# Performance work log

Measured on AMD Instinct MI355X. Metric: run time of the kernel, lower is better.

Reference implementation:

```python
import jax, jax.numpy as jnp
import numpy as np

THETA0 = 3.0
THETA = 5.0


def _edt(bg):
    """Exact Euclidean distance transform.
    bg: [B,H,W] bool, True where distance is 0 (the 'background'/feature set).
    Returns [B,H,W] float32 distance of every pixel to the nearest True pixel.
    Separable two-pass algorithm: 1D pass along H via scan, then exact
    min over column offsets along W (Meijster lower-envelope done densely).
    """
    B, H, W = bg.shape
    big = jnp.float32(H + W)
    f = bg.astype(jnp.float32)
    xs = jnp.moveaxis(f, 1, 0)  # [H,B,W] scan over rows

    def step(carry, row):
        d = jnp.where(row > 0, 0.0, carry + 1.0)
        return d, d

    init = jnp.full((B, W), big, jnp.float32)
    _, gf = jax.lax.scan(step, init, xs)                  # top-down
    _, gb = jax.lax.scan(step, init, xs, reverse=True)    # bottom-up
    g = jnp.minimum(gf, gb)            # [H,B,W] 1D vertical distance
    g = jnp.moveaxis(g, 0, 1)          # [B,H,W]
    g2 = jnp.minimum(g, big) ** 2
    col = jnp.arange(W, dtype=jnp.float32)
    off2 = (col[:, None] - col[None, :]) ** 2             # [j,k]
    # d2[b,i,j] = min_k g2[b,i,k] + (j-k)^2   -> [B,H,W,W] intermediate
    d2 = jnp.min(g2[:, :, None, :] + off2[None, None, :, :], axis=-1)
    return jnp.sqrt(d2)


def reference(predictions, targets):
    # predictions: [B,1,H,W] logits; targets: [B,1,H,W] binary masks
    t = targets[:, 0]                                   # [B,H,W]
    fg = t > 0.5
    dist_pos = _edt(~fg)   # distance_transform_edt(target): dist to nearest 0
    dist_neg = _edt(fg)    # distance_transform_edt(1-target): dist to nearest 1
    dist_map = jnp.where(fg, dist_pos, -dist_neg)
    # weight = 1 / (1 + exp((|d| - theta0)/theta)) == sigmoid(-(|d|-theta0)/theta)
    weight = jax.nn.sigmoid(-(jnp.abs(dist_map) - THETA0) / THETA)[:, None]  # [B,1,H,W]
    # numerically stable BCE-with-logits == BCE(sigmoid(x), t)
    x = predictions
    bce = jnp.maximum(x, 0.0) - x * targets + jnp.log1p(jnp.exp(-jnp.abs(x)))
    return jnp.mean(bce * weight)


def setup_inputs() -> dict:
    key = jax.random.key(0)
    k1, k2 = jax.random.split(key)
    B, C, H, W = 8, 1, 256, 256
    predictions = jax.random.normal(k1, (B, C, H, W), dtype=jnp.float32)
    targets = jax.random.randint(k2, (B, C, H, W), 0, 2).astype(jnp.float32)
    return {"predictions": predictions, "targets": targets}
```

## Files before the change

### kernel.cpp

```cpp
#include <hip/hip_runtime.h>
#include <math.h>

#define BB 8
#define HH 256
#define WW 256
#define NPIX (BB*HH*WW)
#define BIGF 512.0f
#define INF9 1e9f

#define P_OFF   (2 * NPIX)
#define P_STRIDE 32
#define C_OFF   (P_OFF + 16 * P_STRIDE)

__device__ __forceinline__ void col_scan_g2(bool f0, bool f1, bool f2, bool f3,
                                            int lane, float g2[4]) {
  float d = INF9;
  d = f0 ? 0.0f : d + 1.0f; float lf0 = d;
  d = f1 ? 0.0f : d + 1.0f; float lf1 = d;
  d = f2 ? 0.0f : d + 1.0f; float lf2 = d;
  d = f3 ? 0.0f : d + 1.0f; float lf3 = d;
  float F = lf3;
#pragma unroll
  for (int s = 1; s < 64; s <<= 1) {
    float u = __shfl_up(F, s, 64) + 4.0f * (float)s;
    if (lane >= s) F = fminf(F, u);
  }
  float Fe = __shfl_up(F, 1, 64);
  if (lane == 0) Fe = INF9;

  d = INF9;
  d = f3 ? 0.0f : d + 1.0f; float lb3 = d;
  d = f2 ? 0.0f : d + 1.0f; float lb2 = d;
  d = f1 ? 0.0f : d + 1.0f; float lb1 = d;
  d = f0 ? 0.0f : d + 1.0f; float lb0 = d;
  float Bv = lb0;
#pragma unroll
  for (int s = 1; s < 64; s <<= 1) {
    float u = __shfl_down(Bv, s, 64) + 4.0f * (float)s;
    if (lane < 64 - s) Bv = fminf(Bv, u);
  }
  float Be = __shfl_down(Bv, 1, 64);
  if (lane == 63) Be = INF9;

  float v0 = fminf(fminf(lf0, Fe + 1.0f), fminf(lb0, Be + 4.0f));
  float v1 = fminf(fminf(lf1, Fe + 2.0f), fminf(lb1, Be + 3.0f));
  float v2 = fminf(fminf(lf2, Fe + 3.0f), fminf(lb2, Be + 2.0f));
  float v3 = fminf(fminf(lf3, Fe + 4.0f), fminf(lb3, Be + 1.0f));
  v0 = fminf(v0, BIGF); v1 = fminf(v1, BIGF);
  v2 = fminf(v2, BIGF); v3 = fminf(v3, BIGF);
  g2[0] = v0 * v0; g2[1] = v1 * v1; g2[2] = v2 * v2; g2[3] = v3 * v3;
}

__global__ __launch_bounds__(256) void edt_vertical2(
    const float* __restrict__ tgt,
    float* __restrict__ ws) {
  if (blockIdx.x == 0) {
    if (threadIdx.x < 16) ws[P_OFF + threadIdx.x * P_STRIDE] = 0.0f;
    if (threadIdx.x == 16) ((int*)ws)[C_OFF] = 0;
  }

  float* gA2 = ws;
  float* gB2 = ws + NPIX;

  int wid = (blockIdx.x * 256 + threadIdx.x) >> 6;
  int lane = threadIdx.x & 63;
  int b = wid >> 8;
  int w = wid & 255;
  size_t ibase = (size_t)b * HH * WW + w;

  float t0 = tgt[ibase + (size_t)(4 * lane + 0) * WW];
  float t1 = tgt[ibase + (size_t)(4 * lane + 1) * WW];
  float t2 = tgt[ibase + (size_t)(4 * lane + 2) * WW];
  float t3 = tgt[ibase + (size_t)(4 * lane + 3) * WW];
  bool g0 = t0 > 0.5f, g1 = t1 > 0.5f, g2b = t2 > 0.5f, g3 = t3 > 0.5f;

  float a2[4], b2[4];
  col_scan_g2(!g0, !g1, !g2b, !g3, lane, a2);
  col_scan_g2(g0, g1, g2b, g3, lane, b2);

#pragma unroll
  for (int k = 0; k < 4; ++k) {
    size_t o = ibase + (size_t)(4 * lane + k) * WW;
    gA2[o] = a2[k];
    gB2[o] = b2[k];
  }
}

#define ENV_GROUP(kk) { float4 v = s4[kk];                        \
    float D0 = fw - (float)(4 * (kk));                            \
    d2 = fminf(d2, fmaf(D0, D0, v.x));                            \
    float D1 = D0 - 1.0f; d2 = fminf(d2, fmaf(D1, D1, v.y));      \
    float D2 = D0 - 2.0f; d2 = fminf(d2, fmaf(D2, D2, v.z));      \
    float D3 = D0 - 3.0f; d2 = fminf(d2, fmaf(D3, D3, v.w)); }

__global__ __launch_bounds__(1024) void edt_row_loss3(
    const float* __restrict__ pred,
    const float* __restrict__ tgt,
    float* __restrict__ ws,
    float* __restrict__ out) {
  __shared__ __align__(16) float lA[4][WW];
  __shared__ __align__(16) float lB[4][WW];
  __shared__ float wsum[16];
  __shared__ int lastFlag;

  const float* gA2 = ws;
  const float* gB2 = ws + NPIX;
  float* partials = ws + P_OFF;
  int* counter = ((int*)ws) + C_OFF;

  int tid = threadIdx.x;
  size_t base = (size_t)blockIdx.x * (4 * WW);

  ((float*)lA)[tid] = gA2[base + tid];
  ((float*)lB)[tid] = gB2[base + tid];
  float x = pred[base + tid];
  float t = tgt[base + tid];
  __syncthreads();

  int r = tid >> 8;
  int w = tid & 255;
  bool fg = t > 0.5f;
  const float4* s4 = (const float4*)(fg ? lA[r] : lB[r]);

  int w0 = w & ~63;
  int kc0 = w0 >> 2;
  float fw = (float)w;
  float d2 = 1e30f;

#pragma unroll 4
  for (int k = kc0; k < kc0 + 16; ++k) ENV_GROUP(k);

  int kL = kc0 - 1;
  int kR = kc0 + 16;
  for (int iter = 0; iter < 16; ++iter) {
    int bL = (kL >= 0) ? (w0 - 4 * kL - 3) : 100000;
    int bR = (kR <= 63) ? (4 * kR - w0 - 63) : 100000;
    int bb = min(bL, bR);
    float bb2 = (float)bb * (float)bb;
    if (__all(d2 <= bb2)) break;
    if (kL >= 0) { ENV_GROUP(kL); kL--; }
    if (kR <= 63) { ENV_GROUP(kR); kR++; }
  }

  float dd = sqrtf(d2);
  float weight = 1.0f / (1.0f + __expf((dd - 3.0f) * 0.2f));
  float bce = fmaxf(x, 0.0f) - x * t + log1pf(__expf(-fabsf(x)));
  float c = bce * weight * (1.0f / (float)NPIX);

#pragma unroll
  for (int off = 32; off > 0; off >>= 1) c += __shfl_down(c, off, 64);
  if ((tid & 63) == 0) wsum[tid >> 6] = c;
  __syncthreads();

  if (tid < 64) {
    float v = (tid < 16) ? wsum[tid] : 0.0f;
#pragma unroll
    for (int off = 8; off > 0; off >>= 1) v += __shfl_down(v, off, 64);
    if (tid == 0) {
      atomicAdd(&partials[(blockIdx.x & 15) * P_STRIDE], v);
      __threadfence();
      int done = atomicAdd(counter, 1);
      lastFlag = (done == (int)gridDim.x - 1) ? 1 : 0;
    }
  }
  __syncthreads();

  if (lastFlag && tid < 64) {
    float v = (tid < 16) ? atomicAdd(&partials[tid * P_STRIDE], 0.0f) : 0.0f;
#pragma unroll
    for (int off = 8; off > 0; off >>= 1) v += __shfl_down(v, off, 64);
    if (tid == 0) out[0] = v;
  }
}

extern "C" void kernel_launch(void* const* d_in, const int* in_sizes, int n_in,
                              void* d_out, int out_size, void* d_ws, size_t ws_size,
                              hipStream_t stream) {
  const float* pred = (const float*)d_in[0];
  const float* tgt  = (const float*)d_in[1];
  float* out = (float*)d_out;
  float* ws  = (float*)d_ws;

  edt_vertical2<<<dim3(512), dim3(256), 0, stream>>>(tgt, ws);
  edt_row_loss3<<<dim3(512), dim3(1024), 0, stream>>>(pred, tgt, ws, out);
}
```

Measured before the change: 80.82 us.

## Fuse vertical EDT and row-envelope loss into one cooperative kernel with grid sync

Merges the two kernels into a single cooperative launch of 256 blocks of 1024 threads. Each block first does the vertical column scans, with each wave handling one column for one polarity, then hits a grid-wide sync and processes two row-groups of the horizontal envelope plus BCE loss. Prediction and target loads are issued before the sync to hide latency. This removes one kernel launch and its inter-kernel gap, at the cost of a grid barrier and half as many blocks, each doing twice the work.

Measured after the change: 130.6 us. 1.62x slower.

```diff
diff --git a/kernel.cpp b/kernel.cpp
--- a/kernel.cpp
+++ b/kernel.cpp
@@ -1,5 +1,8 @@
 #include <hip/hip_runtime.h>
+#include <hip/hip_cooperative_groups.h>
 #include <math.h>
+
+namespace cg = cooperative_groups;
 
 #define BB 8
 #define HH 256
@@ -51,41 +54,6 @@
   g2[0] = v0 * v0; g2[1] = v1 * v1; g2[2] = v2 * v2; g2[3] = v3 * v3;
 }
 
-__global__ __launch_bounds__(256) void edt_vertical2(
-    const float* __restrict__ tgt,
-    float* __restrict__ ws) {
-  if (blockIdx.x == 0) {
-    if (threadIdx.x < 16) ws[P_OFF + threadIdx.x * P_STRIDE] = 0.0f;
-    if (threadIdx.x == 16) ((int*)ws)[C_OFF] = 0;
-  }
-
-  float* gA2 = ws;
-  float* gB2 = ws + NPIX;
-
-  int wid = (blockIdx.x * 256 + threadIdx.x) >> 6;
-  int lane = threadIdx.x & 63;
-  int b = wid >> 8;
-  int w = wid & 255;
-  size_t ibase = (size_t)b * HH * WW + w;
-
-  float t0 = tgt[ibase + (size_t)(4 * lane + 0) * WW];
-  float t1 = tgt[ibase + (size_t)(4 * lane + 1) * WW];
-  float t2 = tgt[ibase + (size_t)(4 * lane + 2) * WW];
-  float t3 = tgt[ibase + (size_t)(4 * lane + 3) * WW];
-  bool g0 = t0 > 0.5f, g1 = t1 > 0.5f, g2b = t2 > 0.5f, g3 = t3 > 0.5f;
-
-  float a2[4], b2[4];
-  col_scan_g2(!g0, !g1, !g2b, !g3, lane, a2);
-  col_scan_g2(g0, g1, g2b, g3, lane, b2);
-
-#pragma unroll
-  for (int k = 0; k < 4; ++k) {
-    size_t o = ibase + (size_t)(4 * lane + k) * WW;
-    gA2[o] = a2[k];
-    gB2[o] = b2[k];
-  }
-}
-
 #define ENV_GROUP(kk) { float4 v = s4[kk];                        \
     float D0 = fw - (float)(4 * (kk));                            \
     d2 = fminf(d2, fmaf(D0, D0, v.x));                            \
@@ -93,7 +61,7 @@
     float D2 = D0 - 2.0f; d2 = fminf(d2, fmaf(D2, D2, v.z));      \
     float D3 = D0 - 3.0f; d2 = fminf(d2, fmaf(D3, D3, v.w)); }
 
-__global__ __launch_bounds__(1024) void edt_row_loss3(
+__global__ __launch_bounds__(1024) void fused_boundary_loss(
     const float* __restrict__ pred,
     const float* __restrict__ tgt,
     float* __restrict__ ws,
@@ -103,49 +71,106 @@
   __shared__ float wsum[16];
   __shared__ int lastFlag;
 
-  const float* gA2 = ws;
-  const float* gB2 = ws + NPIX;
+  float* gA2 = ws;
+  float* gB2 = ws + NPIX;
   float* partials = ws + P_OFF;
   int* counter = ((int*)ws) + C_OFF;
 
   int tid = threadIdx.x;
-  size_t base = (size_t)blockIdx.x * (4 * WW);
-
-  ((float*)lA)[tid] = gA2[base + tid];
-  ((float*)lB)[tid] = gB2[base + tid];
-  float x = pred[base + tid];
-  float t = tgt[base + tid];
-  __syncthreads();
+
+  if (blockIdx.x == 0) {
+    if (tid < 16) partials[tid * P_STRIDE] = 0.0f;
+    if (tid == 16) *counter = 0;
+  }
+
+  float xx[2], tt[2];
+#pragma unroll
+  for (int it = 0; it < 2; ++it) {
+    size_t base = (size_t)((int)blockIdx.x + (it << 8)) * (4 * WW);
+    xx[it] = pred[base + tid];
+    tt[it] = tgt[base + tid];
+  }
+
+  {
+    int widx = tid >> 6;
+    int lane = tid & 63;
+    int col  = ((int)blockIdx.x << 3) | (widx & 7);
+    int feat = widx >> 3;
+    int b = col >> 8;
+    int w = col & 255;
+    size_t ibase = (size_t)b * (HH * WW) + w;
+
+    float t0 = tgt[ibase + (size_t)(4 * lane + 0) * WW];
+    float t1 = tgt[ibase + (size_t)(4 * lane + 1) * WW];
+    float t2 = tgt[ibase + (size_t)(4 * lane + 2) * WW];
+    float t3 = tgt[ibase + (size_t)(4 * lane + 3) * WW];
+    bool p0 = t0 > 0.5f, p1 = t1 > 0.5f, p2 = t2 > 0.5f, p3 = t3 > 0.5f;
+    bool f0 = feat ? p0 : !p0;
+    bool f1 = feat ? p1 : !p1;
+    bool f2 = feat ? p2 : !p2;
+    bool f3 = feat ? p3 : !p3;
+
+    float g2v[4];
+    col_scan_g2(f0, f1, f2, f3, lane, g2v);
+
+    float* dst = feat ? gB2 : gA2;
+#pragma unroll
+    for (int k = 0; k < 4; ++k)
+      dst[ibase + (size_t)(4 * lane + k) * WW] = g2v[k];
+  }
+
+  cg::this_grid().sync();
 
   int r = tid >> 8;
   int w = tid & 255;
-  bool fg = t > 0.5f;
-  const float4* s4 = (const float4*)(fg ? lA[r] : lB[r]);
-
   int w0 = w & ~63;
   int kc0 = w0 >> 2;
   float fw = (float)w;
-  float d2 = 1e30f;
-
+
+  float la[2], lb[2];
+#pragma unroll
+  for (int it = 0; it < 2; ++it) {
+    size_t base = (size_t)((int)blockIdx.x + (it << 8)) * (4 * WW);
+    la[it] = gA2[base + tid];
+    lb[it] = gB2[base + tid];
+  }
+
+  float acc = 0.0f;
+#pragma unroll
+  for (int it = 0; it < 2; ++it) {
+    __syncthreads();
+    ((float*)lA)[tid] = la[it];
+    ((float*)lB)[tid] = lb[it];
+    __syncthreads();
+
+    float x = xx[it];
+    float t = tt[it];
+    bool fg = t > 0.5f;
+    const float4* s4 = (const float4*)(fg ? lA[r] : lB[r]);
+
+    float d2 = 1e30f;
 #pragma unroll 4
-  for (int k = kc0; k < kc0 + 16; ++k) ENV_GROUP(k);
-
-  int kL = kc0 - 1;
-  int kR = kc0 + 16;
-  for (int iter = 0; iter < 16; ++iter) {
-    int bL = (kL >= 0) ? (w0 - 4 * kL - 3) : 100000;
-    int bR = (kR <= 63) ? (4 * kR - w0 - 63) : 100000;
-    int bb = min(bL, bR);
-    float bb2 = (float)bb * (float)bb;
-    if (__all(d2 <= bb2)) break;
-    if (kL >= 0) { ENV_GROUP(kL); kL--; }
-    if (kR <= 63) { ENV_GROUP(kR); kR++; }
-  }
-
-  float dd = sqrtf(d2);
-  float weight = 1.0f / (1.0f + __expf((dd - 3.0f) * 0.2f));
-  float bce = fmaxf(x, 0.0f) - x * t + log1pf(__expf(-fabsf(x)));
-  float c = bce * weight * (1.0f / (float)NPIX);
+    for (int k = kc0; k < kc0 + 16; ++k) ENV_GROUP(k);
+
+    int kL = kc0 - 1;
+    int kR = kc0 + 16;
+    for (int iter = 0; iter < 16; ++iter) {
+      int bL = (kL >= 0) ? (w0 - 4 * kL - 3) : 100000;
+      int bR = (kR <= 63) ? (4 * kR - w0 - 63) : 100000;
+      int bb = min(bL, bR);
+      float bb2 = (float)bb * (float)bb;
+      if (__all(d2 <= bb2)) break;
+      if (kL >= 0) { ENV_GROUP(kL); kL--; }
+      if (kR <= 63) { ENV_GROUP(kR); kR++; }
+    }
+
+    float dd = sqrtf(d2);
+    float weight = 1.0f / (1.0f + __expf((dd - 3.0f) * 0.2f));
+    float bce = fmaxf(x, 0.0f) - x * t + log1pf(__expf(-fabsf(x)));
+    acc += bce * weight;
+  }
+
+  float c = acc * (1.0f / (float)NPIX);
 
 #pragma unroll
   for (int off = 32; off > 0; off >>= 1) c += __shfl_down(c, off, 64);
@@ -181,6 +206,7 @@
   float* out = (float*)d_out;
   float* ws  = (float*)d_ws;
 
-  edt_vertical2<<<dim3(512), dim3(256), 0, stream>>>(tgt, ws);
-  edt_row_loss3<<<dim3(512), dim3(1024), 0, stream>>>(pred, tgt, ws, out);
+  void* args[] = {(void*)&pred, (void*)&tgt, (void*)&ws, (void*)&out};
+  hipLaunchCooperativeKernel((const void*)fused_boundary_loss,
+                             dim3(256), dim3(1024), args, 0, stream);
 }
```

## Compute vertical EDT pass with column bitmasks and clz/ctz

Applied to the files above, without the earlier changes.

Replaces the shuffle-based prefix-min scan of the vertical distance pass with 32-bit column bitmasks. Each thread packs 32 rows into a mask in shared memory and finds nearest foreground/background distances via count-leading/trailing-zero instructions, carrying across segments. The launch shrinks to 32 blocks of 512 threads, each thread handling 32 rows. This cuts shuffle and float ops but greatly reduces the number of blocks in flight for a memory-bound pass.

Result: faster. 75.88 us (-6.1%).

```diff
diff --git a/kernel.cpp b/kernel.cpp
--- a/kernel.cpp
+++ b/kernel.cpp
@@ -5,55 +5,18 @@
 #define HH 256
 #define WW 256
 #define NPIX (BB*HH*WW)
-#define BIGF 512.0f
-#define INF9 1e9f
+#define BIGI 512
+#define BIGBIG (1<<20)
 
 #define P_OFF   (2 * NPIX)
 #define P_STRIDE 32
 #define C_OFF   (P_OFF + 16 * P_STRIDE)
 
-__device__ __forceinline__ void col_scan_g2(bool f0, bool f1, bool f2, bool f3,
-                                            int lane, float g2[4]) {
-  float d = INF9;
-  d = f0 ? 0.0f : d + 1.0f; float lf0 = d;
-  d = f1 ? 0.0f : d + 1.0f; float lf1 = d;
-  d = f2 ? 0.0f : d + 1.0f; float lf2 = d;
-  d = f3 ? 0.0f : d + 1.0f; float lf3 = d;
-  float F = lf3;
-#pragma unroll
-  for (int s = 1; s < 64; s <<= 1) {
-    float u = __shfl_up(F, s, 64) + 4.0f * (float)s;
-    if (lane >= s) F = fminf(F, u);
-  }
-  float Fe = __shfl_up(F, 1, 64);
-  if (lane == 0) Fe = INF9;
-
-  d = INF9;
-  d = f3 ? 0.0f : d + 1.0f; float lb3 = d;
-  d = f2 ? 0.0f : d + 1.0f; float lb2 = d;
-  d = f1 ? 0.0f : d + 1.0f; float lb1 = d;
-  d = f0 ? 0.0f : d + 1.0f; float lb0 = d;
-  float Bv = lb0;
-#pragma unroll
-  for (int s = 1; s < 64; s <<= 1) {
-    float u = __shfl_down(Bv, s, 64) + 4.0f * (float)s;
-    if (lane < 64 - s) Bv = fminf(Bv, u);
-  }
-  float Be = __shfl_down(Bv, 1, 64);
-  if (lane == 63) Be = INF9;
-
-  float v0 = fminf(fminf(lf0, Fe + 1.0f), fminf(lb0, Be + 4.0f));
-  float v1 = fminf(fminf(lf1, Fe + 2.0f), fminf(lb1, Be + 3.0f));
-  float v2 = fminf(fminf(lf2, Fe + 3.0f), fminf(lb2, Be + 2.0f));
-  float v3 = fminf(fminf(lf3, Fe + 4.0f), fminf(lb3, Be + 1.0f));
-  v0 = fminf(v0, BIGF); v1 = fminf(v1, BIGF);
-  v2 = fminf(v2, BIGF); v3 = fminf(v3, BIGF);
-  g2[0] = v0 * v0; g2[1] = v1 * v1; g2[2] = v2 * v2; g2[3] = v3 * v3;
-}
-
-__global__ __launch_bounds__(256) void edt_vertical2(
+__global__ __launch_bounds__(512) void edt_vertical_bits(
     const float* __restrict__ tgt,
     float* __restrict__ ws) {
+  __shared__ unsigned int smem[8 * 64];
+
   if (blockIdx.x == 0) {
     if (threadIdx.x < 16) ws[P_OFF + threadIdx.x * P_STRIDE] = 0.0f;
     if (threadIdx.x == 16) ((int*)ws)[C_OFF] = 0;
@@ -62,27 +25,70 @@
   float* gA2 = ws;
   float* gB2 = ws + NPIX;
 
-  int wid = (blockIdx.x * 256 + threadIdx.x) >> 6;
-  int lane = threadIdx.x & 63;
-  int b = wid >> 8;
-  int w = wid & 255;
-  size_t ibase = (size_t)b * HH * WW + w;
+  int k = threadIdx.x >> 6;
+  int l = threadIdx.x & 63;
+  int b = blockIdx.x >> 2;
+  int w0 = (blockIdx.x & 3) << 6;
+  size_t ibase = (size_t)b * (HH * WW) + (size_t)w0 + l;
 
-  float t0 = tgt[ibase + (size_t)(4 * lane + 0) * WW];
-  float t1 = tgt[ibase + (size_t)(4 * lane + 1) * WW];
-  float t2 = tgt[ibase + (size_t)(4 * lane + 2) * WW];
-  float t3 = tgt[ibase + (size_t)(4 * lane + 3) * WW];
-  bool g0 = t0 > 0.5f, g1 = t1 > 0.5f, g2b = t2 > 0.5f, g3 = t3 > 0.5f;
+  unsigned int m = 0;
+#pragma unroll
+  for (int i = 0; i < 32; ++i) {
+    float t = tgt[ibase + (size_t)(32 * k + i) * WW];
+    m |= (t > 0.5f ? 1u : 0u) << i;
+  }
+  smem[k * 64 + l] = m;
+  __syncthreads();
 
-  float a2[4], b2[4];
-  col_scan_g2(!g0, !g1, !g2b, !g3, lane, a2);
-  col_scan_g2(g0, g1, g2b, g3, lane, b2);
+  unsigned int Mf[8];
+#pragma unroll
+  for (int j = 0; j < 8; ++j) Mf[j] = smem[j * 64 + l];
 
+  int fcA = BIGBIG, fcB = BIGBIG;
+  {
+    int cA = BIGBIG, cB = BIGBIG;
 #pragma unroll
-  for (int k = 0; k < 4; ++k) {
-    size_t o = ibase + (size_t)(4 * lane + k) * WW;
-    gA2[o] = a2[k];
-    gB2[o] = b2[k];
+    for (int j = 0; j < 8; ++j) {
+      if (j == k) { fcA = cA; fcB = cB; }
+      unsigned int a = ~Mf[j], bm = Mf[j];
+      cA = a  ? (int)__builtin_clz(a)  : cA + 32;
+      cB = bm ? (int)__builtin_clz(bm) : cB + 32;
+    }
+  }
+  int bcA = BIGBIG, bcB = BIGBIG;
+  {
+    int cA = BIGBIG, cB = BIGBIG;
+#pragma unroll
+    for (int j = 7; j >= 0; --j) {
+      if (j == k) { bcA = cA; bcB = cB; }
+      unsigned int a = ~Mf[j], bm = Mf[j];
+      cA = a  ? (int)__builtin_ctz(a)  : cA + 32;
+      cB = bm ? (int)__builtin_ctz(bm) : cB + 32;
+    }
+  }
+
+  unsigned int mB = m;
+  unsigned int mA = ~m;
+  size_t obase = ibase + (size_t)(32 * k) * WW;
+
+#pragma unroll 8
+  for (int rr = 0; rr < 32; ++rr) {
+    {
+      unsigned int x = mA << (31 - rr);
+      unsigned int y = mA >> rr;
+      int df = x ? (int)__builtin_clz(x) : (rr + 1 + fcA);
+      int db = y ? (int)__builtin_ctz(y) : (32 - rr + bcA);
+      int d = min(min(df, db), BIGI);
+      gA2[obase + (size_t)rr * WW] = (float)(d * d);
+    }
+    {
+      unsigned int x = mB << (31 - rr);
+      unsigned int y = mB >> rr;
+      int df = x ? (int)__builtin_clz(x) : (rr + 1 + fcB);
+      int db = y ? (int)__builtin_ctz(y) : (32 - rr + bcB);
+      int d = min(min(df, db), BIGI);
+      gB2[obase + (size_t)rr * WW] = (float)(d * d);
+    }
   }
 }
 
@@ -181,6 +187,6 @@
   float* out = (float*)d_out;
   float* ws  = (float*)d_ws;
 
-  edt_vertical2<<<dim3(512), dim3(256), 0, stream>>>(tgt, ws);
+  edt_vertical_bits<<<dim3(32), dim3(512), 0, stream>>>(tgt, ws);
   edt_row_loss3<<<dim3(512), dim3(1024), 0, stream>>>(pred, tgt, ws, out);
 }
```
